# Kernel optimization log

Measured on AMD Instinct MI355X. Metric: run time of the kernel, lower is better.

The kernel has to match this reference:

```python
import jax, jax.numpy as jnp
import numpy as np

N, S, D_IN, ATTN_DIM, OUT_DIM = 4, 8192, 1024, 1024, 1024


def setup_inputs() -> dict:
    key = jax.random.key(0)
    ks = jax.random.split(key, 6)
    scale_in = 1.0 / np.sqrt(D_IN)
    scale_attn = 1.0 / np.sqrt(ATTN_DIM)
    return {
        "x": jax.random.normal(ks[0], (N, S, D_IN), dtype=jnp.float32),
        "wq": jax.random.normal(ks[1], (D_IN, ATTN_DIM), dtype=jnp.float32) * scale_in,
        "bq": jnp.zeros((ATTN_DIM,), dtype=jnp.float32),
        "wk": jax.random.normal(ks[2], (D_IN, ATTN_DIM), dtype=jnp.float32) * scale_in,
        "bk": jnp.zeros((ATTN_DIM,), dtype=jnp.float32),
        "wv": jax.random.normal(ks[3], (D_IN, ATTN_DIM), dtype=jnp.float32) * scale_in,
        "bv": jnp.zeros((ATTN_DIM,), dtype=jnp.float32),
        "wo": jax.random.normal(ks[4], (ATTN_DIM, OUT_DIM), dtype=jnp.float32) * scale_attn,
        "bo": jnp.zeros((OUT_DIM,), dtype=jnp.float32),
    }


def reference(x, wq, bq, wk, bk, wv, bv, wo, bo):
    # QKV projections (Dense layers)
    query = x @ wq + bq  # [n, s, h]
    key_ = x @ wk + bk
    value = x @ wv + bv
    # elu+1 feature map
    Q = jax.nn.elu(query) + 1.0
    K = jax.nn.elu(key_) + 1.0
    # per-channel global reductions over sequence (einsum 'nsh,nsh->nh')
    KV = jnp.einsum('nsh,nsh->nh', K, value, precision='highest')  # [n, h]
    Ksum = jnp.sum(K, axis=1)  # [n, h]
    Z = 1.0 / (Q * Ksum[:, None, :] + 1e-6)  # [n, s, h]
    V = Q * KV[:, None, :] * Z  # [n, s, h]
    out = V @ wo + bo
    return jax.nn.gelu(out, approximate=True)
```

## Files before the change

### kernel.cpp

```cpp
#include <hip/hip_runtime.h>
#include <math.h>
#include <stdint.h>


#define S_LEN 8192

typedef __attribute__((ext_vector_type(8))) __bf16 bf16x8;
typedef __attribute__((ext_vector_type(8))) unsigned short ushort8;
typedef __attribute__((ext_vector_type(4))) float f32x4;

__device__ __forceinline__ unsigned short f2bf(float f) {
    unsigned int u = __builtin_bit_cast(unsigned int, f);
    unsigned int r = (u + 0x7fffu + ((u >> 16) & 1u)) >> 16;
    return (unsigned short)r;
}
__device__ __forceinline__ float bf2f(unsigned short s) {
    unsigned int u = ((unsigned int)s) << 16;
    return __builtin_bit_cast(float, u);
}
__device__ __forceinline__ float elu1(float v) { return v > 0.f ? v + 1.f : __expf(v); }
__device__ __forceinline__ float gelu_tanh(float v) {
    float u = 1.5957691216057308f * (v + 0.044715f * v * v * v);
    float e = __expf(u);
    float th = 1.f - 2.f / (e + 1.f);
    return 0.5f * v * (1.f + th);
}
__device__ __forceinline__ void glds16(const void* g, void* l) {
    __builtin_amdgcn_global_load_lds(
        (const __attribute__((address_space(1))) unsigned int*)(uintptr_t)g,
        (__attribute__((address_space(3))) unsigned int*)(uintptr_t)l, 16, 0, 0);
}

#define KBAR()  asm volatile("s_barrier" ::: "memory")
#define LGKM0() do { asm volatile("s_waitcnt lgkmcnt(0)" ::: "memory"); \
                     __builtin_amdgcn_sched_barrier(0); } while (0)
#define VM4()   asm volatile("s_waitcnt vmcnt(4)" ::: "memory")
#define VM2()   asm volatile("s_waitcnt vmcnt(2)" ::: "memory")
#define VM0()   asm volatile("s_waitcnt vmcnt(0)" ::: "memory")

#define LDF(P, OFF) __builtin_bit_cast(bf16x8, *(const ushort8*)&(P)[OFF])

__global__ __launch_bounds__(256) void xconv(const float* __restrict__ x,
                                             unsigned short* __restrict__ xb)
{
    const size_t base = ((size_t)blockIdx.x * 256 + threadIdx.x) * 8;
    float4 a = *(const float4*)&x[base];
    float4 b = *(const float4*)&x[base + 4];
    ushort8 o;
    o[0] = f2bf(a.x); o[1] = f2bf(a.y); o[2] = f2bf(a.z); o[3] = f2bf(a.w);
    o[4] = f2bf(b.x); o[5] = f2bf(b.y); o[6] = f2bf(b.z); o[7] = f2bf(b.w);
    *(ushort8*)&xb[base] = o;
}

__global__ __launch_bounds__(256) void wtrans(const float* __restrict__ wq,
                                              const float* __restrict__ wk,
                                              const float* __restrict__ wv,
                                              const float* __restrict__ wo,
                                              unsigned short* __restrict__ wT)
{
    __shared__ float tile[64][65];
    const int z = blockIdx.z;
    const float* w = (z == 0) ? wq : (z == 1) ? wk : (z == 2) ? wv : wo;
    unsigned short* dst = wT + (size_t)z * 1048576;
    const int t  = threadIdx.x;
    const int n0 = blockIdx.x * 64;
    const int k0 = blockIdx.y * 64;
    const int r  = t >> 2;
    const int c4 = (t & 3) * 16;
    #pragma unroll
    for (int j = 0; j < 4; ++j) {
        float4 v = *(const float4*)&w[(size_t)(k0 + r) * 1024 + n0 + c4 + j * 4];
        tile[r][c4 + j * 4 + 0] = v.x; tile[r][c4 + j * 4 + 1] = v.y;
        tile[r][c4 + j * 4 + 2] = v.z; tile[r][c4 + j * 4 + 3] = v.w;
    }
    __syncthreads();
    const int nn = t >> 2;
    const int kc = (t & 3) * 16;
    ushort8 o0, o1;
    #pragma unroll
    for (int j = 0; j < 8; ++j) o0[j] = f2bf(tile[kc + j][nn]);
    #pragma unroll
    for (int j = 0; j < 8; ++j) o1[j] = f2bf(tile[kc + 8 + j][nn]);
    *(ushort8*)&dst[(size_t)(n0 + nn) * 1024 + k0 + kc]     = o0;
    *(ushort8*)&dst[(size_t)(n0 + nn) * 1024 + k0 + kc + 8] = o1;
}

__global__ __launch_bounds__(512) void qkv_mfma(
    const unsigned short* __restrict__ xb,
    const unsigned short* __restrict__ wqT,
    const unsigned short* __restrict__ wkT,
    const unsigned short* __restrict__ wvT,
    const float* __restrict__ bq, const float* __restrict__ bk,
    const float* __restrict__ bv,
    unsigned short* __restrict__ Qout,
    float* __restrict__ KV, float* __restrict__ Ks,
    int moff)
{
    __shared__ unsigned short Alds[3][256 * 64];
    __shared__ unsigned short Blds[2][3][64 * 64];
    __shared__ float redkv[16][64];
    __shared__ float redks[16][64];

    const int t = threadIdx.x;
    const unsigned int nlin = blockIdx.x + 16u * blockIdx.y;
    const unsigned int swz  = (nlin & 7u) * 128u + (nlin >> 3);
    const int h0   = (int)(swz & 15u) * 64;
    const int m0   = (int)(swz >> 4) * 256;
    const int mg   = moff + m0;
    const int bidx = mg >> 13;

    const int lane = t & 63, wid = t >> 6;
    const int wm = wid >> 1, wn = wid & 1;
    const int lr = lane & 15, quad = lane >> 4;

    const int sA   = wid * 64 + lane;
    const int xks0 = ((quad)     ^ (lr & 7)) * 8;
    const int xks1 = ((quad | 4) ^ (lr & 7)) * 8;
    const int arow = (wm * 64 + lr) * 64;
    const int brow = (wn * 32 + lr) * 64;

    auto stA = [&](int kt, int u, int buf) {
        const int s = u * 512 + sA;
        const int r = s >> 3;
        const int j = (s & 7) ^ (r & 7);
        glds16(&xb[(size_t)(m0 + r) * 1024 + kt * 64 + j * 8],
               &Alds[buf][(u * 512 + wid * 64) * 8]);
    };
    auto stB = [&](const unsigned short* w, int mat, int kt, int buf) {
        const int r = sA >> 3;
        const int j = (sA & 7) ^ (r & 7);
        glds16(&w[(size_t)(h0 + r) * 1024 + kt * 64 + j * 8],
               &Blds[buf][mat][wid * 512]);
    };

    f32x4 accq[4][2], acck[4][2], accv[4][2];
    #pragma unroll
    for (int mi = 0; mi < 4; ++mi)
        #pragma unroll
        for (int nj = 0; nj < 2; ++nj) {
            accq[mi][nj] = (f32x4){0.f, 0.f, 0.f, 0.f};
            acck[mi][nj] = (f32x4){0.f, 0.f, 0.f, 0.f};
            accv[mi][nj] = (f32x4){0.f, 0.f, 0.f, 0.f};
        }

    #pragma unroll
    for (int u = 0; u < 4; ++u) stA(0, u, 0);
    stB(wqT, 0, 0, 0); stB(wkT, 1, 0, 0); stB(wvT, 2, 0, 0);
    #pragma unroll
    for (int u = 0; u < 4; ++u) stA(1, u, 1);
    VM4();
    KBAR();

#define QKV_PH(AB, BB, XK, STG, WT)                                             \
    {                                                                           \
        bf16x8 af[4], bmat[3][2];                                               \
        _Pragma("unroll")                                                       \
        for (int mi = 0; mi < 4; ++mi)                                          \
            af[mi] = LDF(Alds[AB], arow + mi * 1024 + (XK));                    \
        _Pragma("unroll")                                                       \
        for (int mt = 0; mt < 3; ++mt)                                          \
            _Pragma("unroll")                                                   \
            for (int nj = 0; nj < 2; ++nj)                                      \
                bmat[mt][nj] = LDF(Blds[BB][mt], brow + nj * 1024 + (XK));      \
        STG;                                                                    \
        KBAR();                                                                 \
        LGKM0();                                                                \
        __builtin_amdgcn_s_setprio(1);                                          \
        _Pragma("unroll")                                                       \
        for (int mi = 0; mi < 4; ++mi)                                          \
            _Pragma("unroll")                                                   \
            for (int nj = 0; nj < 2; ++nj) {                                    \
                accq[mi][nj] = __builtin_amdgcn_mfma_f32_16x16x32_bf16(af[mi], bmat[0][nj], accq[mi][nj], 0, 0, 0); \
                acck[mi][nj] = __builtin_amdgcn_mfma_f32_16x16x32_bf16(af[mi], bmat[1][nj], acck[mi][nj], 0, 0, 0); \
                accv[mi][nj] = __builtin_amdgcn_mfma_f32_16x16x32_bf16(af[mi], bmat[2][nj], accv[mi][nj], 0, 0, 0); \
            }                                                                   \
        __builtin_amdgcn_s_setprio(0);                                          \
        WT;                                                                     \
        KBAR();                                                                 \
    }

    #pragma unroll
    for (int kt = 0; kt < 16; ++kt) {
        const int ab = kt % 3;
        const int bb = kt & 1;
        QKV_PH(ab, bb, xks0,
               {
                   if (kt + 1 < 16) {
                       stB(wqT, 0, kt + 1, (kt + 1) & 1);
                       stB(wkT, 1, kt + 1, (kt + 1) & 1);
                       stB(wvT, 2, kt + 1, (kt + 1) & 1);
                   }
                   if (kt + 2 < 16) {
                       stA(kt + 2, 0, (kt + 2) % 3); stA(kt + 2, 1, (kt + 2) % 3);
                       stA(kt + 2, 2, (kt + 2) % 3); stA(kt + 2, 3, (kt + 2) % 3);
                   }
               },
               {});
        if (kt <= 13) {
            QKV_PH(ab, bb, xks1, {}, VM4());
        } else if (kt == 14) {
            QKV_PH(ab, bb, xks1, {}, VM0());
        } else {
            QKV_PH(ab, bb, xks1, {}, {});
        }
    }
#undef QKV_PH

    float bqv[2], bkv[2], bvv[2];
    #pragma unroll
    for (int nj = 0; nj < 2; ++nj) {
        const int h = h0 + wn * 32 + nj * 16 + lr;
        bqv[nj] = bq[h]; bkv[nj] = bk[h]; bvv[nj] = bv[h];
    }
    float kvp[2] = {0.f, 0.f}, ksp[2] = {0.f, 0.f};
    #pragma unroll
    for (int mi = 0; mi < 4; ++mi)
        #pragma unroll
        for (int nj = 0; nj < 2; ++nj) {
            const int h = h0 + wn * 32 + nj * 16 + lr;
            #pragma unroll
            for (int r = 0; r < 4; ++r) {
                const int m = mg + wm * 64 + mi * 16 + quad * 4 + r;
                float q = elu1(accq[mi][nj][r] + bqv[nj]);
                Qout[(size_t)m * 1024 + h] = f2bf(q);
                float kk = elu1(acck[mi][nj][r] + bkv[nj]);
                float vv = accv[mi][nj][r] + bvv[nj];
                kvp[nj] = fmaf(kk, vv, kvp[nj]);
                ksp[nj] += kk;
            }
        }
    #pragma unroll
    for (int nj = 0; nj < 2; ++nj) {
        redkv[wm * 4 + quad][wn * 32 + nj * 16 + lr] = kvp[nj];
        redks[wm * 4 + quad][wn * 32 + nj * 16 + lr] = ksp[nj];
    }
    __syncthreads();
    if (t < 64) {
        float s = 0.f;
        #pragma unroll
        for (int g = 0; g < 16; ++g) s += redkv[g][t];
        atomicAdd(&KV[bidx * 1024 + h0 + t], s);
    } else if (t < 128) {
        const int c = t - 64;
        float s = 0.f;
        #pragma unroll
        for (int g = 0; g < 16; ++g) s += redks[g][c];
        atomicAdd(&Ks[bidx * 1024 + h0 + c], s);
    }
}

__global__ __launch_bounds__(256) void vprime(
    unsigned short* __restrict__ Q,
    const float* __restrict__ KV, const float* __restrict__ Ks)
{
    const size_t idx  = (size_t)blockIdx.x * 256 + threadIdx.x;
    const size_t base = idx * 8;
    const int h = (int)(base & 1023);
    const int n = (int)(base >> 23);
    ushort8 q8 = *(ushort8*)&Q[base];
    const float* kvp = &KV[n * 1024 + h];
    const float* ksp = &Ks[n * 1024 + h];
    ushort8 o;
    #pragma unroll
    for (int j = 0; j < 8; ++j) {
        float qf = bf2f(q8[j]);
        float vp = qf * kvp[j] * __builtin_amdgcn_rcpf(fmaf(qf, ksp[j], 1e-6f));
        o[j] = f2bf(vp);
    }
    *(ushort8*)&Q[base] = o;
}

__global__ __launch_bounds__(512) void out_mfma(
    const unsigned short* __restrict__ Vp,
    const unsigned short* __restrict__ woT,
    const float* __restrict__ bo, float* __restrict__ out)
{
    __shared__ unsigned short Alds[2][256 * 64];
    __shared__ unsigned short Blds[2][256 * 64];

    const int t  = threadIdx.x;
    const unsigned int nlin = blockIdx.x + 4u * blockIdx.y;
    const unsigned int swz  = (nlin & 7u) * 64u + (nlin >> 3);
    const int h0 = (int)(swz & 3u) * 256;
    const int m0 = (int)(swz >> 2) * 256;

    const int lane = t & 63, wid = t >> 6;
    const int wm = wid >> 2, wn = wid & 3;
    const int lr = lane & 15, quad = lane >> 4;

    const int sA   = wid * 64 + lane;
    const int xks0 = ((quad)     ^ (lr & 7)) * 8;
    const int xks1 = ((quad | 4) ^ (lr & 7)) * 8;
    const int arow = (wm * 128 + lr) * 64;
    const int brow = (wn * 64 + lr) * 64;

    auto stA = [&](int kt, int u, int buf) {
        const int s = u * 512 + sA;
        const int r = s >> 3;
        const int j = (s & 7) ^ (r & 7);
        glds16(&Vp[(size_t)(m0 + r) * 1024 + kt * 64 + j * 8],
               &Alds[buf][(u * 512 + wid * 64) * 8]);
    };
    auto stB = [&](int kt, int u, int buf) {
        const int s = u * 512 + sA;
        const int r = s >> 3;
        const int j = (s & 7) ^ (r & 7);
        glds16(&woT[(size_t)(h0 + r) * 1024 + kt * 64 + j * 8],
               &Blds[buf][(u * 512 + wid * 64) * 8]);
    };

    f32x4 acc[8][4];
    #pragma unroll
    for (int mr = 0; mr < 8; ++mr)
        #pragma unroll
        for (int nc = 0; nc < 4; ++nc) acc[mr][nc] = (f32x4){0.f, 0.f, 0.f, 0.f};

    #pragma unroll
    for (int u = 0; u < 4; ++u) stA(0, u, 0);
    #pragma unroll
    for (int u = 0; u < 4; ++u) stB(0, u, 0);
    stA(1, 0, 1); stA(1, 1, 1);
    VM2();
    KBAR();

    bf16x8 af[4][2], bf_[2][2];

#define OUT_LDA(BUF, MH)                                                        \
    {                                                                           \
        _Pragma("unroll")                                                       \
        for (int mi = 0; mi < 4; ++mi) {                                        \
            af[mi][0] = __builtin_bit_cast(bf16x8,                              \
                *(const ushort8*)&Alds[BUF][arow + (MH) * 4096 + mi * 1024 + xks0]); \
            af[mi][1] = __builtin_bit_cast(bf16x8,                              \
                *(const ushort8*)&Alds[BUF][arow + (MH) * 4096 + mi * 1024 + xks1]); \
        }                                                                       \
    }

#define OUT_LDB(BUF, NH)                                                        \
    {                                                                           \
        _Pragma("unroll")                                                       \
        for (int nj = 0; nj < 2; ++nj) {                                        \
            bf_[nj][0] = __builtin_bit_cast(bf16x8,                             \
                *(const ushort8*)&Blds[BUF][brow + (NH) * 2048 + nj * 1024 + xks0]); \
            bf_[nj][1] = __builtin_bit_cast(bf16x8,                             \
                *(const ushort8*)&Blds[BUF][brow + (NH) * 2048 + nj * 1024 + xks1]); \
        }                                                                       \
    }

#define OUT_PHASE(MH, NH, STG, WT)                                              \
    {                                                                           \
        STG;                                                                    \
        KBAR();                                                                 \
        LGKM0();                                                                \
        __builtin_amdgcn_s_setprio(1);                                          \
        _Pragma("unroll")                                                       \
        for (int mi = 0; mi < 4; ++mi)                                          \
            _Pragma("unroll")                                                   \
            for (int nj = 0; nj < 2; ++nj) {                                    \
                acc[(MH) * 4 + mi][(NH) * 2 + nj] = __builtin_amdgcn_mfma_f32_16x16x32_bf16( \
                    af[mi][0], bf_[nj][0], acc[(MH) * 4 + mi][(NH) * 2 + nj], 0, 0, 0); \
                acc[(MH) * 4 + mi][(NH) * 2 + nj] = __builtin_amdgcn_mfma_f32_16x16x32_bf16( \
                    af[mi][1], bf_[nj][1], acc[(MH) * 4 + mi][(NH) * 2 + nj], 0, 0, 0); \
            }                                                                   \
        __builtin_amdgcn_s_setprio(0);                                          \
        WT;                                                                     \
        KBAR();                                                                 \
    }

    for (int i = 0; i < 8; ++i) {
        const int t1 = 2 * i + 1;
        OUT_LDA(0, 0); OUT_LDB(0, 0);
        OUT_PHASE(0, 0, { stA(t1, 2, 1); stA(t1, 3, 1); }, {});
        OUT_LDB(0, 1);
        OUT_PHASE(0, 1, { stB(t1, 0, 1); stB(t1, 1, 1); }, {});
        OUT_LDA(0, 1);
        OUT_PHASE(1, 1, { stB(t1, 2, 1); stB(t1, 3, 1); }, {});
        OUT_LDB(0, 0);
        if (i < 7) {
            OUT_PHASE(1, 0, { stA(t1 + 1, 0, 0); stA(t1 + 1, 1, 0); }, VM2());
        } else {
            OUT_PHASE(1, 0, {}, VM0());
        }
        OUT_LDA(1, 0); OUT_LDB(1, 0);
        if (i < 7) {
            OUT_PHASE(0, 0, { stA(t1 + 1, 2, 0); stA(t1 + 1, 3, 0); }, {});
            OUT_LDB(1, 1);
            OUT_PHASE(0, 1, { stB(t1 + 1, 0, 0); stB(t1 + 1, 1, 0); }, {});
            OUT_LDA(1, 1);
            OUT_PHASE(1, 1, { stB(t1 + 1, 2, 0); stB(t1 + 1, 3, 0); }, {});
            OUT_LDB(1, 0);
            OUT_PHASE(1, 0, { stA(t1 + 2, 0, 1); stA(t1 + 2, 1, 1); }, VM2());
        } else {
            OUT_PHASE(0, 0, {}, {});
            OUT_LDB(1, 1);
            OUT_PHASE(0, 1, {}, {});
            OUT_LDA(1, 1);
            OUT_PHASE(1, 1, {}, {});
            OUT_LDB(1, 0);
            OUT_PHASE(1, 0, {}, {});
        }
    }
#undef OUT_LDA
#undef OUT_LDB
#undef OUT_PHASE

    float bov[4];
    #pragma unroll
    for (int nc = 0; nc < 4; ++nc) bov[nc] = bo[h0 + wn * 64 + nc * 16 + lr];
    #pragma unroll
    for (int mr = 0; mr < 8; ++mr)
        #pragma unroll
        for (int nc = 0; nc < 4; ++nc) {
            const int h = h0 + wn * 64 + nc * 16 + lr;
            #pragma unroll
            for (int r = 0; r < 4; ++r) {
                const int m = m0 + wm * 128 + mr * 16 + quad * 4 + r;
                out[(size_t)m * 1024 + h] = gelu_tanh(acc[mr][nc][r] + bov[nc]);
            }
        }
}

extern "C" void kernel_launch(void* const* d_in, const int* in_sizes, int n_in,
                              void* d_out, int out_size, void* d_ws, size_t ws_size,
                              hipStream_t stream)
{
    const float* x  = (const float*)d_in[0];
    const float* wq = (const float*)d_in[1];
    const float* bq = (const float*)d_in[2];
    const float* wk = (const float*)d_in[3];
    const float* bk = (const float*)d_in[4];
    const float* wv = (const float*)d_in[5];
    const float* bv = (const float*)d_in[6];
    const float* wo = (const float*)d_in[7];
    const float* bo = (const float*)d_in[8];
    float* out = (float*)d_out;

    char* wsb = (char*)d_ws;
    unsigned short* Qws = (unsigned short*)wsb;
    unsigned short* xb  = (unsigned short*)(wsb + 67108864ULL);
    unsigned short* wqT = (unsigned short*)(wsb + 100663296ULL);
    unsigned short* wkT = wqT + 1048576;
    unsigned short* wvT = wkT + 1048576;
    unsigned short* woT = wvT + 1048576;
    float* KV = (float*)(wsb + 100663296ULL + 4ULL * 2097152);
    float* Ks = KV + 4 * 1024;

    hipMemsetAsync(KV, 0, 2 * 4 * 1024 * sizeof(float), stream);

    wtrans<<<dim3(16, 16, 4), 256, 0, stream>>>(wq, wk, wv, wo, wqT);

    for (int half = 0; half < 2; ++half) {
        xconv<<<8192, 256, 0, stream>>>(x + (size_t)half * 16384 * 1024, xb);
        qkv_mfma<<<dim3(16, 64), 512, 0, stream>>>(xb, wqT, wkT, wvT, bq, bk, bv,
                                                   Qws, KV, Ks, half * 16384);
    }
    vprime<<<16384, 256, 0, stream>>>(Qws, KV, Ks);
    out_mfma<<<dim3(4, 128), 512, 0, stream>>>(Qws, woT, bo, out);
}
```

Baseline: 524.7 us.

## Restructure GEMM main loops to one barrier per k-tile with triple-buffered A

Both the QKV and output-projection GEMM loops drop the multi-phase, barrier-heavy schedule in favour of one barrier per k-tile. Each iteration issues all LDS fragment reads for the tile, launches global-to-LDS prefetches in between, then runs all MFMAs back to back. The output kernel now triple-buffers its A tile in LDS so prefetch runs two tiles ahead, and the explicit lgkmcnt waits and sched barriers are gone, leaving wait placement to the compiler. The aim is to cut synchronisation overhead, at the cost of more LDS and registers, which may lower occupancy and interleave LDS reads less finely with MFMA.

```diff
diff --git a/kernel.cpp b/kernel.cpp
--- a/kernel.cpp
+++ b/kernel.cpp
@@ -32,10 +32,7 @@
 }
 
 #define KBAR()  asm volatile("s_barrier" ::: "memory")
-#define LGKM0() do { asm volatile("s_waitcnt lgkmcnt(0)" ::: "memory"); \
-                     __builtin_amdgcn_sched_barrier(0); } while (0)
 #define VM4()   asm volatile("s_waitcnt vmcnt(4)" ::: "memory")
-#define VM2()   asm volatile("s_waitcnt vmcnt(2)" ::: "memory")
 #define VM0()   asm volatile("s_waitcnt vmcnt(0)" ::: "memory")
 
 #define LDF(P, OFF) __builtin_bit_cast(bf16x8, *(const ushort8*)&(P)[OFF])
@@ -151,60 +148,60 @@
     VM4();
     KBAR();
 
-#define QKV_PH(AB, BB, XK, STG, WT)                                             \
-    {                                                                           \
-        bf16x8 af[4], bmat[3][2];                                               \
-        _Pragma("unroll")                                                       \
-        for (int mi = 0; mi < 4; ++mi)                                          \
-            af[mi] = LDF(Alds[AB], arow + mi * 1024 + (XK));                    \
-        _Pragma("unroll")                                                       \
-        for (int mt = 0; mt < 3; ++mt)                                          \
-            _Pragma("unroll")                                                   \
-            for (int nj = 0; nj < 2; ++nj)                                      \
-                bmat[mt][nj] = LDF(Blds[BB][mt], brow + nj * 1024 + (XK));      \
-        STG;                                                                    \
-        KBAR();                                                                 \
-        LGKM0();                                                                \
-        __builtin_amdgcn_s_setprio(1);                                          \
-        _Pragma("unroll")                                                       \
-        for (int mi = 0; mi < 4; ++mi)                                          \
-            _Pragma("unroll")                                                   \
-            for (int nj = 0; nj < 2; ++nj) {                                    \
-                accq[mi][nj] = __builtin_amdgcn_mfma_f32_16x16x32_bf16(af[mi], bmat[0][nj], accq[mi][nj], 0, 0, 0); \
-                acck[mi][nj] = __builtin_amdgcn_mfma_f32_16x16x32_bf16(af[mi], bmat[1][nj], acck[mi][nj], 0, 0, 0); \
-                accv[mi][nj] = __builtin_amdgcn_mfma_f32_16x16x32_bf16(af[mi], bmat[2][nj], accv[mi][nj], 0, 0, 0); \
-            }                                                                   \
-        __builtin_amdgcn_s_setprio(0);                                          \
-        WT;                                                                     \
-        KBAR();                                                                 \
-    }
-
     #pragma unroll
     for (int kt = 0; kt < 16; ++kt) {
         const int ab = kt % 3;
         const int bb = kt & 1;
-        QKV_PH(ab, bb, xks0,
-               {
-                   if (kt + 1 < 16) {
-                       stB(wqT, 0, kt + 1, (kt + 1) & 1);
-                       stB(wkT, 1, kt + 1, (kt + 1) & 1);
-                       stB(wvT, 2, kt + 1, (kt + 1) & 1);
-                   }
-                   if (kt + 2 < 16) {
-                       stA(kt + 2, 0, (kt + 2) % 3); stA(kt + 2, 1, (kt + 2) % 3);
-                       stA(kt + 2, 2, (kt + 2) % 3); stA(kt + 2, 3, (kt + 2) % 3);
-                   }
-               },
-               {});
-        if (kt <= 13) {
-            QKV_PH(ab, bb, xks1, {}, VM4());
-        } else if (kt == 14) {
-            QKV_PH(ab, bb, xks1, {}, VM0());
-        } else {
-            QKV_PH(ab, bb, xks1, {}, {});
-        }
-    }
-#undef QKV_PH
+        bf16x8 af0[4], af1[4], b0[3][2], b1[3][2];
+        #pragma unroll
+        for (int mi = 0; mi < 4; ++mi)
+            af0[mi] = LDF(Alds[ab], arow + mi * 1024 + xks0);
+        #pragma unroll
+        for (int mt = 0; mt < 3; ++mt)
+            #pragma unroll
+            for (int nj = 0; nj < 2; ++nj)
+                b0[mt][nj] = LDF(Blds[bb][mt], brow + nj * 1024 + xks0);
+        if (kt + 1 < 16) {
+            stB(wqT, 0, kt + 1, (kt + 1) & 1);
+            stB(wkT, 1, kt + 1, (kt + 1) & 1);
+            stB(wvT, 2, kt + 1, (kt + 1) & 1);
+        }
+        if (kt + 2 < 16) {
+            stA(kt + 2, 0, (kt + 2) % 3); stA(kt + 2, 1, (kt + 2) % 3);
+            stA(kt + 2, 2, (kt + 2) % 3); stA(kt + 2, 3, (kt + 2) % 3);
+        }
+        #pragma unroll
+        for (int mi = 0; mi < 4; ++mi)
+            af1[mi] = LDF(Alds[ab], arow + mi * 1024 + xks1);
+        #pragma unroll
+        for (int mt = 0; mt < 3; ++mt)
+            #pragma unroll
+            for (int nj = 0; nj < 2; ++nj)
+                b1[mt][nj] = LDF(Blds[bb][mt], brow + nj * 1024 + xks1);
+
+        __builtin_amdgcn_s_setprio(1);
+        #pragma unroll
+        for (int mi = 0; mi < 4; ++mi)
+            #pragma unroll
+            for (int nj = 0; nj < 2; ++nj) {
+                accq[mi][nj] = __builtin_amdgcn_mfma_f32_16x16x32_bf16(af0[mi], b0[0][nj], accq[mi][nj], 0, 0, 0);
+                acck[mi][nj] = __builtin_amdgcn_mfma_f32_16x16x32_bf16(af0[mi], b0[1][nj], acck[mi][nj], 0, 0, 0);
+                accv[mi][nj] = __builtin_amdgcn_mfma_f32_16x16x32_bf16(af0[mi], b0[2][nj], accv[mi][nj], 0, 0, 0);
+            }
+        #pragma unroll
+        for (int mi = 0; mi < 4; ++mi)
+            #pragma unroll
+            for (int nj = 0; nj < 2; ++nj) {
+                accq[mi][nj] = __builtin_amdgcn_mfma_f32_16x16x32_bf16(af1[mi], b1[0][nj], accq[mi][nj], 0, 0, 0);
+                acck[mi][nj] = __builtin_amdgcn_mfma_f32_16x16x32_bf16(af1[mi], b1[1][nj], acck[mi][nj], 0, 0, 0);
+                accv[mi][nj] = __builtin_amdgcn_mfma_f32_16x16x32_bf16(af1[mi], b1[2][nj], accv[mi][nj], 0, 0, 0);
+            }
+        __builtin_amdgcn_s_setprio(0);
+
+        if (kt <= 13)      VM4();
+        else if (kt == 14) VM0();
+        if (kt < 15) KBAR();
+    }
 
     float bqv[2], bkv[2], bvv[2];
     #pragma unroll
@@ -275,7 +272,7 @@
     const unsigned short* __restrict__ woT,
     const float* __restrict__ bo, float* __restrict__ out)
 {
-    __shared__ unsigned short Alds[2][256 * 64];
+    __shared__ unsigned short Alds[3][256 * 64];
     __shared__ unsigned short Blds[2][256 * 64];
 
     const int t  = threadIdx.x;
@@ -319,90 +316,60 @@
     for (int u = 0; u < 4; ++u) stA(0, u, 0);
     #pragma unroll
     for (int u = 0; u < 4; ++u) stB(0, u, 0);
-    stA(1, 0, 1); stA(1, 1, 1);
-    VM2();
+    #pragma unroll
+    for (int u = 0; u < 4; ++u) stA(1, u, 1);
+    VM4();
     KBAR();
 
-    bf16x8 af[4][2], bf_[2][2];
-
-#define OUT_LDA(BUF, MH)                                                        \
-    {                                                                           \
-        _Pragma("unroll")                                                       \
-        for (int mi = 0; mi < 4; ++mi) {                                        \
-            af[mi][0] = __builtin_bit_cast(bf16x8,                              \
-                *(const ushort8*)&Alds[BUF][arow + (MH) * 4096 + mi * 1024 + xks0]); \
-            af[mi][1] = __builtin_bit_cast(bf16x8,                              \
-                *(const ushort8*)&Alds[BUF][arow + (MH) * 4096 + mi * 1024 + xks1]); \
-        }                                                                       \
-    }
-
-#define OUT_LDB(BUF, NH)                                                        \
-    {                                                                           \
-        _Pragma("unroll")                                                       \
-        for (int nj = 0; nj < 2; ++nj) {                                        \
-            bf_[nj][0] = __builtin_bit_cast(bf16x8,                             \
-                *(const ushort8*)&Blds[BUF][brow + (NH) * 2048 + nj * 1024 + xks0]); \
-            bf_[nj][1] = __builtin_bit_cast(bf16x8,                             \
-                *(const ushort8*)&Blds[BUF][brow + (NH) * 2048 + nj * 1024 + xks1]); \
-        }                                                                       \
-    }
-
-#define OUT_PHASE(MH, NH, STG, WT)                                              \
-    {                                                                           \
-        STG;                                                                    \
-        KBAR();                                                                 \
-        LGKM0();                                                                \
-        __builtin_amdgcn_s_setprio(1);                                          \
-        _Pragma("unroll")                                                       \
-        for (int mi = 0; mi < 4; ++mi)                                          \
-            _Pragma("unroll")                                                   \
-            for (int nj = 0; nj < 2; ++nj) {                                    \
-                acc[(MH) * 4 + mi][(NH) * 2 + nj] = __builtin_amdgcn_mfma_f32_16x16x32_bf16( \
-                    af[mi][0], bf_[nj][0], acc[(MH) * 4 + mi][(NH) * 2 + nj], 0, 0, 0); \
-                acc[(MH) * 4 + mi][(NH) * 2 + nj] = __builtin_amdgcn_mfma_f32_16x16x32_bf16( \
-                    af[mi][1], bf_[nj][1], acc[(MH) * 4 + mi][(NH) * 2 + nj], 0, 0, 0); \
-            }                                                                   \
-        __builtin_amdgcn_s_setprio(0);                                          \
-        WT;                                                                     \
-        KBAR();                                                                 \
-    }
-
-    for (int i = 0; i < 8; ++i) {
-        const int t1 = 2 * i + 1;
-        OUT_LDA(0, 0); OUT_LDB(0, 0);
-        OUT_PHASE(0, 0, { stA(t1, 2, 1); stA(t1, 3, 1); }, {});
-        OUT_LDB(0, 1);
-        OUT_PHASE(0, 1, { stB(t1, 0, 1); stB(t1, 1, 1); }, {});
-        OUT_LDA(0, 1);
-        OUT_PHASE(1, 1, { stB(t1, 2, 1); stB(t1, 3, 1); }, {});
-        OUT_LDB(0, 0);
-        if (i < 7) {
-            OUT_PHASE(1, 0, { stA(t1 + 1, 0, 0); stA(t1 + 1, 1, 0); }, VM2());
-        } else {
-            OUT_PHASE(1, 0, {}, VM0());
-        }
-        OUT_LDA(1, 0); OUT_LDB(1, 0);
-        if (i < 7) {
-            OUT_PHASE(0, 0, { stA(t1 + 1, 2, 0); stA(t1 + 1, 3, 0); }, {});
-            OUT_LDB(1, 1);
-            OUT_PHASE(0, 1, { stB(t1 + 1, 0, 0); stB(t1 + 1, 1, 0); }, {});
-            OUT_LDA(1, 1);
-            OUT_PHASE(1, 1, { stB(t1 + 1, 2, 0); stB(t1 + 1, 3, 0); }, {});
-            OUT_LDB(1, 0);
-            OUT_PHASE(1, 0, { stA(t1 + 2, 0, 1); stA(t1 + 2, 1, 1); }, VM2());
-        } else {
-            OUT_PHASE(0, 0, {}, {});
-            OUT_LDB(1, 1);
-            OUT_PHASE(0, 1, {}, {});
-            OUT_LDA(1, 1);
-            OUT_PHASE(1, 1, {}, {});
-            OUT_LDB(1, 0);
-            OUT_PHASE(1, 0, {}, {});
-        }
-    }
-#undef OUT_LDA
-#undef OUT_LDB
-#undef OUT_PHASE
+    #pragma unroll
+    for (int kt = 0; kt < 16; ++kt) {
+        const int ab = kt % 3;
+        const int bb = kt & 1;
+        bf16x8 af[2][8], bfr[2][4];
+        #pragma unroll
+        for (int mh = 0; mh < 2; ++mh)
+            #pragma unroll
+            for (int mi = 0; mi < 4; ++mi)
+                af[0][mh * 4 + mi] = LDF(Alds[ab], arow + mh * 4096 + mi * 1024 + xks0);
+        #pragma unroll
+        for (int nh = 0; nh < 2; ++nh)
+            #pragma unroll
+            for (int nj = 0; nj < 2; ++nj)
+                bfr[0][nh * 2 + nj] = LDF(Blds[bb], brow + nh * 2048 + nj * 1024 + xks0);
+        if (kt + 1 < 16) {
+            stB(kt + 1, 0, (kt + 1) & 1); stB(kt + 1, 1, (kt + 1) & 1);
+            stB(kt + 1, 2, (kt + 1) & 1); stB(kt + 1, 3, (kt + 1) & 1);
+        }
+        if (kt + 2 < 16) {
+            stA(kt + 2, 0, (kt + 2) % 3); stA(kt + 2, 1, (kt + 2) % 3);
+            stA(kt + 2, 2, (kt + 2) % 3); stA(kt + 2, 3, (kt + 2) % 3);
+        }
+        #pragma unroll
+        for (int mh = 0; mh < 2; ++mh)
+            #pragma unroll
+            for (int mi = 0; mi < 4; ++mi)
+                af[1][mh * 4 + mi] = LDF(Alds[ab], arow + mh * 4096 + mi * 1024 + xks1);
+        #pragma unroll
+        for (int nh = 0; nh < 2; ++nh)
+            #pragma unroll
+            for (int nj = 0; nj < 2; ++nj)
+                bfr[1][nh * 2 + nj] = LDF(Blds[bb], brow + nh * 2048 + nj * 1024 + xks1);
+
+        __builtin_amdgcn_s_setprio(1);
+        #pragma unroll
+        for (int s = 0; s < 2; ++s)
+            #pragma unroll
+            for (int mr = 0; mr < 8; ++mr)
+                #pragma unroll
+                for (int nc = 0; nc < 4; ++nc)
+                    acc[mr][nc] = __builtin_amdgcn_mfma_f32_16x16x32_bf16(
+                        af[s][mr], bfr[s][nc], acc[mr][nc], 0, 0, 0);
+        __builtin_amdgcn_s_setprio(0);
+
+        if (kt <= 13)      VM4();
+        else if (kt == 14) VM0();
+        if (kt < 15) KBAR();
+    }
 
     float bov[4];
     #pragma unroll
```

New measurement: 517.0 us. Within noise of the previous version (-1.5%).
